# Performance work log

Hardware: AMD Instinct MI355X
Metric: run time of the kernel (lower is better)

Reference implementation:

```python
import jax, jax.numpy as jnp
import numpy as np

NUM_GRAPHS = 1000


def setup_inputs() -> dict:
    key = jax.random.key(0)
    ks = jax.random.split(key, 8)
    N, E, F_IN, H = 100000, 1600000, 128, 64
    x = jax.random.normal(ks[0], (N, F_IN), dtype=jnp.float32)
    edge_index = jax.random.randint(ks[1], (2, E), 0, N, dtype=jnp.int64)
    batch = jnp.sort(jax.random.randint(ks[2], (N,), 0, NUM_GRAPHS, dtype=jnp.int64))
    # Glorot-ish scaled weights
    W1 = jax.random.normal(ks[3], (F_IN, H), dtype=jnp.float32) / np.sqrt(F_IN)
    W2 = jax.random.normal(ks[4], (H, H), dtype=jnp.float32) / np.sqrt(H)
    W3 = jax.random.normal(ks[5], (H, H), dtype=jnp.float32) / np.sqrt(H)
    Wl = jax.random.normal(ks[6], (H, 1), dtype=jnp.float32) / np.sqrt(H)
    return {
        "x": x, "edge_index": edge_index, "batch": batch,
        "W1": W1, "b1": jnp.zeros((H,), jnp.float32),
        "W2": W2, "b2": jnp.zeros((H,), jnp.float32),
        "W3": W3, "b3": jnp.zeros((H,), jnp.float32),
        "Wl": Wl, "bl": jnp.zeros((1,), jnp.float32),
    }


def _gcn_prep(edge_index, n_nodes):
    """Add self-loops and compute symmetric normalization coefficients."""
    loops = jnp.arange(n_nodes, dtype=edge_index.dtype)
    src = jnp.concatenate([edge_index[0], loops])  # [E+N]
    dst = jnp.concatenate([edge_index[1], loops])  # [E+N]
    deg = jax.ops.segment_sum(jnp.ones_like(dst, dtype=jnp.float32), dst,
                              num_segments=n_nodes)
    dinv = jnp.where(deg > 0, jax.lax.rsqrt(jnp.maximum(deg, 1.0)), 0.0)
    norm = dinv[src] * dinv[dst]  # [E+N]
    return src, dst, norm


def _gcn_conv(h, W, b, src, dst, norm, n_nodes):
    h = h @ W                              # [N, H] linear transform first
    msg = h[src] * norm[:, None]           # gather + normalize
    agg = jax.ops.segment_sum(msg, dst, num_segments=n_nodes)  # scatter-add
    return agg + b


def reference(x, edge_index, batch, W1, b1, W2, b2, W3, b3, Wl, bl):
    n_nodes = x.shape[0]
    src, dst, norm = _gcn_prep(edge_index, n_nodes)
    h = jax.nn.relu(_gcn_conv(x, W1, b1, src, dst, norm, n_nodes))
    h = jax.nn.relu(_gcn_conv(h, W2, b2, src, dst, norm, n_nodes))
    h = _gcn_conv(h, W3, b3, src, dst, norm, n_nodes)
    # global_mean_pool over graphs
    sums = jax.ops.segment_sum(h, batch, num_segments=NUM_GRAPHS)
    cnts = jax.ops.segment_sum(jnp.ones((n_nodes,), jnp.float32), batch,
                               num_segments=NUM_GRAPHS)
    pooled = sums / jnp.maximum(cnts, 1.0)[:, None]
    # dropout is identity in eval mode
    return pooled @ Wl + bl
```

## Files before the change

### kernel.cpp

```cpp
#include <hip/hip_runtime.h>
#include <stdint.h>

#define BKT 1024
#define EPB 4096

typedef __attribute__((ext_vector_type(8))) __bf16 bf16x8;
typedef __attribute__((ext_vector_type(4))) float floatx4;

__device__ __forceinline__ float bf2f(unsigned short h) {
    return __uint_as_float(((unsigned)h) << 16);
}
__device__ __forceinline__ float4 bf4(ushort4 v) {
    return make_float4(bf2f(v.x), bf2f(v.y), bf2f(v.z), bf2f(v.w));
}
__device__ __forceinline__ unsigned short f2bf(float f) {
    unsigned u = __float_as_uint(f);
    u = u + 0x7FFFu + ((u >> 16) & 1u);
    return (unsigned short)(u >> 16);
}
__device__ __forceinline__ ushort4 pack4(float a, float b, float c, float d) {
    ushort4 r; r.x = f2bf(a); r.y = f2bf(b); r.z = f2bf(c); r.w = f2bf(d); return r;
}


__global__ __launch_bounds__(256) void coarse_hist(const int* __restrict__ dst,
                                                   int* __restrict__ coarse, int E, int NBK) {
    __shared__ int h[128];
    if (threadIdx.x < 128) h[threadIdx.x] = 0;
    __syncthreads();
    int stride = gridDim.x * 256;
    for (int i = blockIdx.x * 256 + threadIdx.x; i < E; i += stride)
        atomicAdd(&h[dst[i] >> 10], 1);
    __syncthreads();
    if (threadIdx.x < NBK) {
        int v = h[threadIdx.x];
        if (v) atomicAdd(&coarse[threadIdx.x], v);
    }
}

__global__ void coarse_scan(const int* __restrict__ coarse, int* __restrict__ bbase,
                            int NBK, int E) {
    if (threadIdx.x == 0 && blockIdx.x == 0) {
        int run = 0;
        for (int i = 0; i < NBK; ++i) { bbase[i] = run; run += coarse[i]; }
        bbase[NBK] = E;
    }
}


__global__ __launch_bounds__(256) void partition_kernel(const int* __restrict__ src,
                                                        const int* __restrict__ dst,
                                                        const int* __restrict__ bbase,
                                                        int* __restrict__ gbcur,
                                                        int2* __restrict__ pairs,
                                                        int E, int NBK) {
    __shared__ int2 stage[EPB];
    __shared__ int  hist[128], offs[129], gbase[128], lcur[128];
    int base = blockIdx.x * EPB;
    int cntE = min(EPB, E - base);
    if (threadIdx.x < 128) hist[threadIdx.x] = 0;
    __syncthreads();
    for (int i = threadIdx.x; i < cntE; i += 256) {
        int b = dst[base + i] >> 10;
        atomicAdd(&hist[b], 1);
    }
    __syncthreads();
    if (threadIdx.x == 0) {
        int run = 0;
        for (int b = 0; b < NBK; ++b) { offs[b] = run; run += hist[b]; }
        offs[NBK] = run;
    }
    __syncthreads();
    if (threadIdx.x < NBK) {
        int b = threadIdx.x;
        int h = hist[b];
        if (h > 0) gbase[b] = bbase[b] + atomicAdd(&gbcur[b << 4], h);
        lcur[b] = offs[b];
    }
    __syncthreads();
    for (int i = threadIdx.x; i < cntE; i += 256) {
        int e = base + i;
        int d = dst[e];
        int b = d >> 10;
        int slot = atomicAdd(&lcur[b], 1);
        stage[slot] = make_int2(src[e], d);
    }
    __syncthreads();
    int total = offs[NBK];
    for (int j = threadIdx.x; j < total; j += 256) {
        int lo = 0, hi = NBK;
        while (lo < hi) { int mid = (lo + hi) >> 1; if (offs[mid + 1] <= j) lo = mid + 1; else hi = mid; }
        pairs[gbase[lo] + (j - offs[lo])] = stage[j];
    }
}


__global__ __launch_bounds__(256) void bucket_build(const int2* __restrict__ pairs,
                                                    const int* __restrict__ bbase,
                                                    int* __restrict__ rowptr,
                                                    int* __restrict__ csr, int N, int E) {
    __shared__ int cnt[BKT];
    __shared__ int psum[256];
    int b = blockIdx.x;
    int nbase = b << 10;
    int pbeg = bbase[b], pend = bbase[b + 1];
    for (int i = threadIdx.x; i < BKT; i += 256) cnt[i] = 0;
    __syncthreads();
    for (int j = pbeg + (int)threadIdx.x; j < pend; j += 256)
        atomicAdd(&cnt[pairs[j].y - nbase], 1);
    __syncthreads();
    int i0 = threadIdx.x * 4;
    int c0 = cnt[i0], c1 = cnt[i0 + 1], c2 = cnt[i0 + 2], c3 = cnt[i0 + 3];
    int local = c0 + c1 + c2 + c3;
    psum[threadIdx.x] = local;
    __syncthreads();
    for (int d = 1; d < 256; d <<= 1) {
        int t = (threadIdx.x >= d) ? psum[threadIdx.x - d] : 0;
        __syncthreads();
        psum[threadIdx.x] += t;
        __syncthreads();
    }
    int excl = psum[threadIdx.x] - local;
    int o0 = pbeg + excl;
    int o1 = o0 + c0, o2 = o1 + c1, o3 = o2 + c2;
    int n0 = nbase + i0;
    if (n0 < N)     rowptr[n0]     = o0;
    if (n0 + 1 < N) rowptr[n0 + 1] = o1;
    if (n0 + 2 < N) rowptr[n0 + 2] = o2;
    if (n0 + 3 < N) rowptr[n0 + 3] = o3;
    cnt[i0] = o0; cnt[i0 + 1] = o1; cnt[i0 + 2] = o2; cnt[i0 + 3] = o3;
    __syncthreads();
    for (int j = pbeg + (int)threadIdx.x; j < pend; j += 256) {
        int2 p = pairs[j];
        int slot = atomicAdd(&cnt[p.y - nbase], 1);
        csr[slot] = p.x;
    }
    if (b == 0 && threadIdx.x == 0) rowptr[N] = E;
}


__global__ __launch_bounds__(256) void gemm1_mfma(const float* __restrict__ X,
                                                  const float* __restrict__ W,
                                                  const int* __restrict__ rowptr,
                                                  __bf16* __restrict__ gbh, int N) {
    __shared__ __align__(16) __bf16 Wt[64][136];
    for (int i = threadIdx.x; i < 128 * 64; i += 256) {
        int k = i >> 6, c = i & 63;
        Wt[c][k] = (__bf16)W[i];
    }
    __syncthreads();

    int wave = threadIdx.x >> 6;
    int l = threadIdx.x & 63;
    int cidx = l & 15;
    int g = l >> 4;
    int wbase = blockIdx.x * 64 + wave * 16;

    int arow = wbase + cidx;
    int arowc = min(arow, N - 1);
    const float4* xr = (const float4*)(X + (size_t)arowc * 128);
    bf16x8 afr[4];
#pragma unroll
    for (int kb = 0; kb < 4; ++kb) {
        float4 p = xr[kb * 8 + g * 2];
        float4 q = xr[kb * 8 + g * 2 + 1];
        bf16x8 a;
        a[0] = (__bf16)p.x; a[1] = (__bf16)p.y; a[2] = (__bf16)p.z; a[3] = (__bf16)p.w;
        a[4] = (__bf16)q.x; a[5] = (__bf16)q.y; a[6] = (__bf16)q.z; a[7] = (__bf16)q.w;
        afr[kb] = a;
    }

    floatx4 acc[4];
#pragma unroll
    for (int ct = 0; ct < 4; ++ct) acc[ct] = (floatx4){0.f, 0.f, 0.f, 0.f};

#pragma unroll
    for (int ct = 0; ct < 4; ++ct) {
#pragma unroll
        for (int kb = 0; kb < 4; ++kb) {
            bf16x8 bfr = *(const bf16x8*)&Wt[ct * 16 + cidx][kb * 32 + g * 8];
            acc[ct] = __builtin_amdgcn_mfma_f32_16x16x32_bf16(afr[kb], bfr, acc[ct], 0, 0, 0);
        }
    }

    int r0 = wbase + g * 4;
    int rp[5];
#pragma unroll
    for (int i = 0; i < 5; ++i) rp[i] = rowptr[min(r0 + i, N)];
#pragma unroll
    for (int i = 0; i < 4; ++i) {
        int row = r0 + i;
        if (row < N) {
            float dv = rsqrtf((float)(rp[i + 1] - rp[i]) + 1.0f);
#pragma unroll
            for (int ct = 0; ct < 4; ++ct)
                gbh[(size_t)row * 64 + ct * 16 + cidx] = (__bf16)(acc[ct][i] * dv);
        }
    }
}


__global__ __launch_bounds__(256) void fused_layer_kernel(const ushort4* __restrict__ gb,
                                                          const int* __restrict__ rowptr,
                                                          const int* __restrict__ csr,
                                                          const float* __restrict__ bias,
                                                          const float* __restrict__ W,
                                                          ushort4* __restrict__ out, int N) {
    __shared__ float Ws[64 * 64];
    __shared__ float T[16][72];
    {
        const float4* Wv = (const float4*)W;
        float4* Wsv = (float4*)Ws;
        for (int i = threadIdx.x; i < 64 * 16; i += 256) Wsv[i] = Wv[i];
    }
    int row = threadIdx.x >> 4;
    int node = blockIdx.x * 16 + row;
    int t = threadIdx.x & 15;
    int c = t * 4;
    float dinv = 0.f;
    if (node < N) {
        int beg = rowptr[node], end = rowptr[node + 1];
        dinv = rsqrtf((float)(end - beg) + 1.0f);
        float4 acc = bf4(gb[(size_t)node * 16 + t]);
        int j = beg;
        for (; j + 8 <= end; j += 8) {
            int s0 = csr[j], s1 = csr[j + 1], s2 = csr[j + 2], s3 = csr[j + 3];
            int s4 = csr[j + 4], s5 = csr[j + 5], s6 = csr[j + 6], s7 = csr[j + 7];
            float4 v0 = bf4(gb[(size_t)s0 * 16 + t]);
            float4 v1 = bf4(gb[(size_t)s1 * 16 + t]);
            float4 v2 = bf4(gb[(size_t)s2 * 16 + t]);
            float4 v3 = bf4(gb[(size_t)s3 * 16 + t]);
            float4 v4 = bf4(gb[(size_t)s4 * 16 + t]);
            float4 v5 = bf4(gb[(size_t)s5 * 16 + t]);
            float4 v6 = bf4(gb[(size_t)s6 * 16 + t]);
            float4 v7 = bf4(gb[(size_t)s7 * 16 + t]);
            acc.x += ((v0.x + v1.x) + (v2.x + v3.x)) + ((v4.x + v5.x) + (v6.x + v7.x));
            acc.y += ((v0.y + v1.y) + (v2.y + v3.y)) + ((v4.y + v5.y) + (v6.y + v7.y));
            acc.z += ((v0.z + v1.z) + (v2.z + v3.z)) + ((v4.z + v5.z) + (v6.z + v7.z));
            acc.w += ((v0.w + v1.w) + (v2.w + v3.w)) + ((v4.w + v5.w) + (v6.w + v7.w));
        }
        for (; j + 2 <= end; j += 2) {
            int s0 = csr[j], s1 = csr[j + 1];
            float4 v0 = bf4(gb[(size_t)s0 * 16 + t]);
            float4 v1 = bf4(gb[(size_t)s1 * 16 + t]);
            acc.x += v0.x + v1.x; acc.y += v0.y + v1.y;
            acc.z += v0.z + v1.z; acc.w += v0.w + v1.w;
        }
        if (j < end) {
            int s0 = csr[j];
            float4 v0 = bf4(gb[(size_t)s0 * 16 + t]);
            acc.x += v0.x; acc.y += v0.y; acc.z += v0.z; acc.w += v0.w;
        }
        float4 bb = *(const float4*)&bias[c];
        T[row][c + 0] = fmaxf(acc.x * dinv + bb.x, 0.f);
        T[row][c + 1] = fmaxf(acc.y * dinv + bb.y, 0.f);
        T[row][c + 2] = fmaxf(acc.z * dinv + bb.z, 0.f);
        T[row][c + 3] = fmaxf(acc.w * dinv + bb.w, 0.f);
    }
    __syncthreads();
    if (node >= N) return;
    float4 o = make_float4(0.f, 0.f, 0.f, 0.f);
#pragma unroll 16
    for (int k = 0; k < 64; ++k) {
        float tv = T[row][k];
        float4 wv = *(const float4*)&Ws[k * 64 + c];
        o.x += tv * wv.x; o.y += tv * wv.y;
        o.z += tv * wv.z; o.w += tv * wv.w;
    }
    out[(size_t)node * 16 + t] = pack4(o.x * dinv, o.y * dinv, o.z * dinv, o.w * dinv);
}


__global__ __launch_bounds__(256) void agg_dot_kernel(const ushort4* __restrict__ gb,
                                                      const int* __restrict__ rowptr,
                                                      const int* __restrict__ csr,
                                                      const float* __restrict__ bias,
                                                      const float* __restrict__ Wl,
                                                      float* __restrict__ s_node, int N) {
    int tid = blockIdx.x * blockDim.x + threadIdx.x;
    int node = tid >> 4;
    if (node >= N) return;
    int t = tid & 15;
    int beg = rowptr[node], end = rowptr[node + 1];
    float dinv = rsqrtf((float)(end - beg) + 1.0f);
    float4 acc = bf4(gb[(size_t)node * 16 + t]);
    int j = beg;
    for (; j + 8 <= end; j += 8) {
        int s0 = csr[j], s1 = csr[j + 1], s2 = csr[j + 2], s3 = csr[j + 3];
        int s4 = csr[j + 4], s5 = csr[j + 5], s6 = csr[j + 6], s7 = csr[j + 7];
        float4 v0 = bf4(gb[(size_t)s0 * 16 + t]);
        float4 v1 = bf4(gb[(size_t)s1 * 16 + t]);
        float4 v2 = bf4(gb[(size_t)s2 * 16 + t]);
        float4 v3 = bf4(gb[(size_t)s3 * 16 + t]);
        float4 v4 = bf4(gb[(size_t)s4 * 16 + t]);
        float4 v5 = bf4(gb[(size_t)s5 * 16 + t]);
        float4 v6 = bf4(gb[(size_t)s6 * 16 + t]);
        float4 v7 = bf4(gb[(size_t)s7 * 16 + t]);
        acc.x += ((v0.x + v1.x) + (v2.x + v3.x)) + ((v4.x + v5.x) + (v6.x + v7.x));
        acc.y += ((v0.y + v1.y) + (v2.y + v3.y)) + ((v4.y + v5.y) + (v6.y + v7.y));
        acc.z += ((v0.z + v1.z) + (v2.z + v3.z)) + ((v4.z + v5.z) + (v6.z + v7.z));
        acc.w += ((v0.w + v1.w) + (v2.w + v3.w)) + ((v4.w + v5.w) + (v6.w + v7.w));
    }
    for (; j + 2 <= end; j += 2) {
        int s0 = csr[j], s1 = csr[j + 1];
        float4 v0 = bf4(gb[(size_t)s0 * 16 + t]);
        float4 v1 = bf4(gb[(size_t)s1 * 16 + t]);
        acc.x += v0.x + v1.x; acc.y += v0.y + v1.y;
        acc.z += v0.z + v1.z; acc.w += v0.w + v1.w;
    }
    if (j < end) {
        int s0 = csr[j];
        float4 v0 = bf4(gb[(size_t)s0 * 16 + t]);
        acc.x += v0.x; acc.y += v0.y; acc.z += v0.z; acc.w += v0.w;
    }
    float4 bb = *(const float4*)&bias[t * 4];
    float4 wl = *(const float4*)&Wl[t * 4];
    float s = (acc.x * dinv + bb.x) * wl.x + (acc.y * dinv + bb.y) * wl.y +
              (acc.z * dinv + bb.z) * wl.z + (acc.w * dinv + bb.w) * wl.w;
    s += __shfl_xor(s, 1);
    s += __shfl_xor(s, 2);
    s += __shfl_xor(s, 4);
    s += __shfl_xor(s, 8);
    if (t == 0) s_node[node] = s;
}


__device__ __forceinline__ int lower_bound_dev(const int* __restrict__ a, int n, int v) {
    int lo = 0, hi = n;
    while (lo < hi) { int mid = (lo + hi) >> 1; if (a[mid] < v) lo = mid + 1; else hi = mid; }
    return lo;
}

__global__ void pool_out_kernel(const float* __restrict__ s_node, const int* __restrict__ batch,
                                const float* __restrict__ bl, float* __restrict__ out, int N) {
    int gidx = blockIdx.x;
    int lo = lower_bound_dev(batch, N, gidx);
    int hi = lower_bound_dev(batch, N, gidx + 1);
    float s = 0.f;
    for (int i = lo + threadIdx.x; i < hi; i += 64) s += s_node[i];
    for (int d = 32; d; d >>= 1) s += __shfl_down(s, d);
    if (threadIdx.x == 0) out[gidx] = s / fmaxf((float)(hi - lo), 1.0f) + bl[0];
}


extern "C" void kernel_launch(void* const* d_in, const int* in_sizes, int n_in,
                              void* d_out, int out_size, void* d_ws, size_t ws_size,
                              hipStream_t stream) {
    const float* x   = (const float*)d_in[0];
    const int*   ei  = (const int*)d_in[1];
    const int*   bat = (const int*)d_in[2];
    const float* W1  = (const float*)d_in[3];
    const float* b1  = (const float*)d_in[4];
    const float* W2  = (const float*)d_in[5];
    const float* b2  = (const float*)d_in[6];
    const float* W3  = (const float*)d_in[7];
    const float* b3  = (const float*)d_in[8];
    const float* Wl  = (const float*)d_in[9];
    const float* bl  = (const float*)d_in[10];

    const int N = in_sizes[0] / 128;
    const int E = in_sizes[1] / 2;
    const int G = out_size;

    const int* src = ei;
    const int* dst = ei + E;

    const int NBK = (N + BKT - 1) / BKT;
    const int Np = (N + 4) & ~3;

    int*     rowptr = (int*)d_ws;
    int*     coarse = rowptr + Np;
    int*     bbase  = coarse + 128;
    int*     gbcur  = bbase + 132;
    int*     csr    = gbcur + (size_t)NBK * 16;
    int2*    pairs  = (int2*)(csr + E);
    ushort4* gbA    = (ushort4*)(pairs + E);
    ushort4* gbB    = gbA + (size_t)N * 16;
    float*   s_node = (float*)(gbB + (size_t)N * 16);

    hipMemsetAsync(coarse, 0, (260 + (size_t)NBK * 16) * sizeof(int), stream);
    coarse_hist<<<256, 256, 0, stream>>>(dst, coarse, E, NBK);
    coarse_scan<<<1, 64, 0, stream>>>(coarse, bbase, NBK, E);
    partition_kernel<<<(E + EPB - 1) / EPB, 256, 0, stream>>>(src, dst, bbase, gbcur, pairs, E, NBK);
    bucket_build<<<NBK, 256, 0, stream>>>(pairs, bbase, rowptr, csr, N, E);

    const int tileGrid = (N + 15) / 16;
    const int aggGrid  = (int)(((size_t)N * 16 + 255) / 256);

    gemm1_mfma<<<(N + 63) / 64, 256, 0, stream>>>(x, W1, rowptr, (__bf16*)gbA, N);
    fused_layer_kernel<<<tileGrid, 256, 0, stream>>>(gbA, rowptr, csr, b1, W2, gbB, N);
    fused_layer_kernel<<<tileGrid, 256, 0, stream>>>(gbB, rowptr, csr, b2, W3, gbA, N);
    agg_dot_kernel<<<aggGrid, 256, 0, stream>>>(gbA, rowptr, csr, b3, Wl, s_node, N);
    pool_out_kernel<<<G, 64, 0, stream>>>(s_node, bat, bl, (float*)d_out, N);
}
```

Before: 280.2 us.

## Project final layer onto output weight before aggregation to gather scalars

Uses linearity of the last GCN layer and the pooling to apply Wl before neighbor aggregation. The second fused layer now emits a per-node scalar instead of a 64-wide bf16 row, and a new scalar aggregation kernel gathers single floats per edge. The b3·Wl term is folded into the pooling kernel. This removes the wide gather traffic of the final layer. It slightly changes semantics for empty graphs, where the bias dot is still added.

Measured after the change: 245.4 us. 1.14x faster.

```diff
diff --git a/kernel.cpp b/kernel.cpp
--- a/kernel.cpp
+++ b/kernel.cpp
@@ -200,12 +200,15 @@
 }
 
 
+template <bool WRITE_P>
 __global__ __launch_bounds__(256) void fused_layer_kernel(const ushort4* __restrict__ gb,
                                                           const int* __restrict__ rowptr,
                                                           const int* __restrict__ csr,
                                                           const float* __restrict__ bias,
                                                           const float* __restrict__ W,
-                                                          ushort4* __restrict__ out, int N) {
+                                                          ushort4* __restrict__ out,
+                                                          const float* __restrict__ Wl,
+                                                          float* __restrict__ p, int N) {
     __shared__ float Ws[64 * 64];
     __shared__ float T[16][72];
     {
@@ -267,61 +270,36 @@
         o.x += tv * wv.x; o.y += tv * wv.y;
         o.z += tv * wv.z; o.w += tv * wv.w;
     }
-    out[(size_t)node * 16 + t] = pack4(o.x * dinv, o.y * dinv, o.z * dinv, o.w * dinv);
-}
-
-
-__global__ __launch_bounds__(256) void agg_dot_kernel(const ushort4* __restrict__ gb,
-                                                      const int* __restrict__ rowptr,
-                                                      const int* __restrict__ csr,
-                                                      const float* __restrict__ bias,
-                                                      const float* __restrict__ Wl,
-                                                      float* __restrict__ s_node, int N) {
-    int tid = blockIdx.x * blockDim.x + threadIdx.x;
-    int node = tid >> 4;
-    if (node >= N) return;
-    int t = tid & 15;
-    int beg = rowptr[node], end = rowptr[node + 1];
+    if (WRITE_P) {
+        float4 wl = *(const float4*)&Wl[c];
+        float s = (o.x * wl.x + o.y * wl.y) + (o.z * wl.z + o.w * wl.w);
+        s += __shfl_xor(s, 1);
+        s += __shfl_xor(s, 2);
+        s += __shfl_xor(s, 4);
+        s += __shfl_xor(s, 8);
+        if (t == 0) p[node] = s * dinv;
+    } else {
+        out[(size_t)node * 16 + t] = pack4(o.x * dinv, o.y * dinv, o.z * dinv, o.w * dinv);
+    }
+}
+
+
+__global__ __launch_bounds__(256) void scalar_agg(const float* __restrict__ p,
+                                                  const int* __restrict__ rowptr,
+                                                  const int* __restrict__ csr,
+                                                  float* __restrict__ s_node, int N) {
+    int n = blockIdx.x * 256 + threadIdx.x;
+    if (n >= N) return;
+    int beg = rowptr[n], end = rowptr[n + 1];
     float dinv = rsqrtf((float)(end - beg) + 1.0f);
-    float4 acc = bf4(gb[(size_t)node * 16 + t]);
+    float acc = p[n];
     int j = beg;
-    for (; j + 8 <= end; j += 8) {
-        int s0 = csr[j], s1 = csr[j + 1], s2 = csr[j + 2], s3 = csr[j + 3];
-        int s4 = csr[j + 4], s5 = csr[j + 5], s6 = csr[j + 6], s7 = csr[j + 7];
-        float4 v0 = bf4(gb[(size_t)s0 * 16 + t]);
-        float4 v1 = bf4(gb[(size_t)s1 * 16 + t]);
-        float4 v2 = bf4(gb[(size_t)s2 * 16 + t]);
-        float4 v3 = bf4(gb[(size_t)s3 * 16 + t]);
-        float4 v4 = bf4(gb[(size_t)s4 * 16 + t]);
-        float4 v5 = bf4(gb[(size_t)s5 * 16 + t]);
-        float4 v6 = bf4(gb[(size_t)s6 * 16 + t]);
-        float4 v7 = bf4(gb[(size_t)s7 * 16 + t]);
-        acc.x += ((v0.x + v1.x) + (v2.x + v3.x)) + ((v4.x + v5.x) + (v6.x + v7.x));
-        acc.y += ((v0.y + v1.y) + (v2.y + v3.y)) + ((v4.y + v5.y) + (v6.y + v7.y));
-        acc.z += ((v0.z + v1.z) + (v2.z + v3.z)) + ((v4.z + v5.z) + (v6.z + v7.z));
-        acc.w += ((v0.w + v1.w) + (v2.w + v3.w)) + ((v4.w + v5.w) + (v6.w + v7.w));
-    }
-    for (; j + 2 <= end; j += 2) {
-        int s0 = csr[j], s1 = csr[j + 1];
-        float4 v0 = bf4(gb[(size_t)s0 * 16 + t]);
-        float4 v1 = bf4(gb[(size_t)s1 * 16 + t]);
-        acc.x += v0.x + v1.x; acc.y += v0.y + v1.y;
-        acc.z += v0.z + v1.z; acc.w += v0.w + v1.w;
-    }
-    if (j < end) {
-        int s0 = csr[j];
-        float4 v0 = bf4(gb[(size_t)s0 * 16 + t]);
-        acc.x += v0.x; acc.y += v0.y; acc.z += v0.z; acc.w += v0.w;
-    }
-    float4 bb = *(const float4*)&bias[t * 4];
-    float4 wl = *(const float4*)&Wl[t * 4];
-    float s = (acc.x * dinv + bb.x) * wl.x + (acc.y * dinv + bb.y) * wl.y +
-              (acc.z * dinv + bb.z) * wl.z + (acc.w * dinv + bb.w) * wl.w;
-    s += __shfl_xor(s, 1);
-    s += __shfl_xor(s, 2);
-    s += __shfl_xor(s, 4);
-    s += __shfl_xor(s, 8);
-    if (t == 0) s_node[node] = s;
+    for (; j + 4 <= end; j += 4) {
+        float a0 = p[csr[j]], a1 = p[csr[j + 1]], a2 = p[csr[j + 2]], a3 = p[csr[j + 3]];
+        acc += (a0 + a1) + (a2 + a3);
+    }
+    for (; j < end; ++j) acc += p[csr[j]];
+    s_node[n] = acc * dinv;
 }
 
 
@@ -332,14 +310,20 @@
 }
 
 __global__ void pool_out_kernel(const float* __restrict__ s_node, const int* __restrict__ batch,
+                                const float* __restrict__ b3, const float* __restrict__ Wl,
                                 const float* __restrict__ bl, float* __restrict__ out, int N) {
+    float v = b3[threadIdx.x] * Wl[threadIdx.x];
+    for (int d = 32; d; d >>= 1) v += __shfl_down(v, d);
+    float bldot = __shfl(v, 0, 64);
+
     int gidx = blockIdx.x;
     int lo = lower_bound_dev(batch, N, gidx);
     int hi = lower_bound_dev(batch, N, gidx + 1);
     float s = 0.f;
     for (int i = lo + threadIdx.x; i < hi; i += 64) s += s_node[i];
     for (int d = 32; d; d >>= 1) s += __shfl_down(s, d);
-    if (threadIdx.x == 0) out[gidx] = s / fmaxf((float)(hi - lo), 1.0f) + bl[0];
+    if (threadIdx.x == 0)
+        out[gidx] = s / fmaxf((float)(hi - lo), 1.0f) + bldot + bl[0];
 }
 
 
@@ -376,7 +360,8 @@
     int2*    pairs  = (int2*)(csr + E);
     ushort4* gbA    = (ushort4*)(pairs + E);
     ushort4* gbB    = gbA + (size_t)N * 16;
-    float*   s_node = (float*)(gbB + (size_t)N * 16);
+    float*   pbuf   = (float*)(gbB + (size_t)N * 16);
+    float*   s_node = pbuf + N;
 
     hipMemsetAsync(coarse, 0, (260 + (size_t)NBK * 16) * sizeof(int), stream);
     coarse_hist<<<256, 256, 0, stream>>>(dst, coarse, E, NBK);
@@ -385,11 +370,10 @@
     bucket_build<<<NBK, 256, 0, stream>>>(pairs, bbase, rowptr, csr, N, E);
 
     const int tileGrid = (N + 15) / 16;
-    const int aggGrid  = (int)(((size_t)N * 16 + 255) / 256);
 
     gemm1_mfma<<<(N + 63) / 64, 256, 0, stream>>>(x, W1, rowptr, (__bf16*)gbA, N);
-    fused_layer_kernel<<<tileGrid, 256, 0, stream>>>(gbA, rowptr, csr, b1, W2, gbB, N);
-    fused_layer_kernel<<<tileGrid, 256, 0, stream>>>(gbB, rowptr, csr, b2, W3, gbA, N);
-    agg_dot_kernel<<<aggGrid, 256, 0, stream>>>(gbA, rowptr, csr, b3, Wl, s_node, N);
-    pool_out_kernel<<<G, 64, 0, stream>>>(s_node, bat, bl, (float*)d_out, N);
-}
+    fused_layer_kernel<false><<<tileGrid, 256, 0, stream>>>(gbA, rowptr, csr, b1, W2, gbB, nullptr, nullptr, N);
+    fused_layer_kernel<true><<<tileGrid, 256, 0, stream>>>(gbB, rowptr, csr, b2, W3, nullptr, Wl, pbuf, N);
+    scalar_agg<<<(N + 255) / 256, 256, 0, stream>>>(pbuf, rowptr, csr, s_node, N);
+    pool_out_kernel<<<G, 64, 0, stream>>>(s_node, bat, b3, Wl, bl, (float*)d_out, N);
+}
```

## Fold W3·Wl into scalar projection and aggregate layer 3 as scalars

Applied to the files above, without the earlier changes.

The third GCN layer is linear, so W3 and Wl are combined into a 64-vector. Layer 2 is aggregated with ReLU and projected onto that vector, giving one scalar per node. Layer 3's neighbour aggregation then becomes a scalar gather instead of a full 64-wide bf16 gather, and b3·Wl is added in the pooling kernel. This removes one full fused layer (a 64-wide aggregate plus GEMM) at the cost of two small kernels. The histogram loops also switch to int4 loads of dst.

New measurement: 232.4 us (median of 2 runs). -17.1%, faster.

```diff
diff --git a/kernel.cpp b/kernel.cpp
--- a/kernel.cpp
+++ b/kernel.cpp
@@ -23,13 +23,33 @@
 }
 
 
+__global__ void w3l_kernel(const float* __restrict__ W3, const float* __restrict__ Wl,
+                           float* __restrict__ w3l) {
+    int k = threadIdx.x;
+    float s = 0.f;
+#pragma unroll 16
+    for (int c = 0; c < 64; ++c) s += W3[k * 64 + c] * Wl[c];
+    w3l[k] = s;
+}
+
+
 __global__ __launch_bounds__(256) void coarse_hist(const int* __restrict__ dst,
                                                    int* __restrict__ coarse, int E, int NBK) {
     __shared__ int h[128];
     if (threadIdx.x < 128) h[threadIdx.x] = 0;
     __syncthreads();
     int stride = gridDim.x * 256;
-    for (int i = blockIdx.x * 256 + threadIdx.x; i < E; i += stride)
+    int gid = blockIdx.x * 256 + threadIdx.x;
+    const int4* d4 = (const int4*)dst;
+    int E4 = E >> 2;
+    for (int i = gid; i < E4; i += stride) {
+        int4 v = d4[i];
+        atomicAdd(&h[v.x >> 10], 1);
+        atomicAdd(&h[v.y >> 10], 1);
+        atomicAdd(&h[v.z >> 10], 1);
+        atomicAdd(&h[v.w >> 10], 1);
+    }
+    for (int i = (E4 << 2) + gid; i < E; i += stride)
         atomicAdd(&h[dst[i] >> 10], 1);
     __syncthreads();
     if (threadIdx.x < NBK) {
@@ -60,9 +80,18 @@
     int cntE = min(EPB, E - base);
     if (threadIdx.x < 128) hist[threadIdx.x] = 0;
     __syncthreads();
-    for (int i = threadIdx.x; i < cntE; i += 256) {
-        int b = dst[base + i] >> 10;
-        atomicAdd(&hist[b], 1);
+    {
+        const int4* d4 = (const int4*)(dst + base);
+        int c4 = cntE >> 2;
+        for (int i = threadIdx.x; i < c4; i += 256) {
+            int4 v = d4[i];
+            atomicAdd(&hist[v.x >> 10], 1);
+            atomicAdd(&hist[v.y >> 10], 1);
+            atomicAdd(&hist[v.z >> 10], 1);
+            atomicAdd(&hist[v.w >> 10], 1);
+        }
+        for (int i = (c4 << 2) + (int)threadIdx.x; i < cntE; i += 256)
+            atomicAdd(&hist[dst[base + i] >> 10], 1);
     }
     __syncthreads();
     if (threadIdx.x == 0) {
@@ -271,12 +300,12 @@
 }
 
 
-__global__ __launch_bounds__(256) void agg_dot_kernel(const ushort4* __restrict__ gb,
-                                                      const int* __restrict__ rowptr,
-                                                      const int* __restrict__ csr,
-                                                      const float* __restrict__ bias,
-                                                      const float* __restrict__ Wl,
-                                                      float* __restrict__ s_node, int N) {
+__global__ __launch_bounds__(256) void agg_dot2_kernel(const ushort4* __restrict__ gb,
+                                                       const int* __restrict__ rowptr,
+                                                       const int* __restrict__ csr,
+                                                       const float* __restrict__ bias,
+                                                       const float* __restrict__ w3l,
+                                                       float* __restrict__ p, int N) {
     int tid = blockIdx.x * blockDim.x + threadIdx.x;
     int node = tid >> 4;
     if (node >= N) return;
@@ -314,14 +343,36 @@
         acc.x += v0.x; acc.y += v0.y; acc.z += v0.z; acc.w += v0.w;
     }
     float4 bb = *(const float4*)&bias[t * 4];
-    float4 wl = *(const float4*)&Wl[t * 4];
-    float s = (acc.x * dinv + bb.x) * wl.x + (acc.y * dinv + bb.y) * wl.y +
-              (acc.z * dinv + bb.z) * wl.z + (acc.w * dinv + bb.w) * wl.w;
+    float4 wv = *(const float4*)&w3l[t * 4];
+    float hx = fmaxf(acc.x * dinv + bb.x, 0.f);
+    float hy = fmaxf(acc.y * dinv + bb.y, 0.f);
+    float hz = fmaxf(acc.z * dinv + bb.z, 0.f);
+    float hw = fmaxf(acc.w * dinv + bb.w, 0.f);
+    float s = (hx * wv.x + hy * wv.y) + (hz * wv.z + hw * wv.w);
     s += __shfl_xor(s, 1);
     s += __shfl_xor(s, 2);
     s += __shfl_xor(s, 4);
     s += __shfl_xor(s, 8);
-    if (t == 0) s_node[node] = s;
+    if (t == 0) p[node] = s * dinv;
+}
+
+
+__global__ __launch_bounds__(256) void scalar_agg(const float* __restrict__ p,
+                                                  const int* __restrict__ rowptr,
+                                                  const int* __restrict__ csr,
+                                                  float* __restrict__ s_node, int N) {
+    int n = blockIdx.x * 256 + threadIdx.x;
+    if (n >= N) return;
+    int beg = rowptr[n], end = rowptr[n + 1];
+    float dinv = rsqrtf((float)(end - beg) + 1.0f);
+    float acc = p[n];
+    int j = beg;
+    for (; j + 4 <= end; j += 4) {
+        float a0 = p[csr[j]], a1 = p[csr[j + 1]], a2 = p[csr[j + 2]], a3 = p[csr[j + 3]];
+        acc += (a0 + a1) + (a2 + a3);
+    }
+    for (; j < end; ++j) acc += p[csr[j]];
+    s_node[n] = acc * dinv;
 }
 
 
@@ -332,14 +383,20 @@
 }
 
 __global__ void pool_out_kernel(const float* __restrict__ s_node, const int* __restrict__ batch,
+                                const float* __restrict__ b3, const float* __restrict__ Wl,
                                 const float* __restrict__ bl, float* __restrict__ out, int N) {
+    float v = b3[threadIdx.x] * Wl[threadIdx.x];
+    for (int d = 32; d; d >>= 1) v += __shfl_down(v, d);
+    float bldot = __shfl(v, 0, 64);
+
     int gidx = blockIdx.x;
     int lo = lower_bound_dev(batch, N, gidx);
     int hi = lower_bound_dev(batch, N, gidx + 1);
     float s = 0.f;
     for (int i = lo + threadIdx.x; i < hi; i += 64) s += s_node[i];
     for (int d = 32; d; d >>= 1) s += __shfl_down(s, d);
-    if (threadIdx.x == 0) out[gidx] = s / fmaxf((float)(hi - lo), 1.0f) + bl[0];
+    if (threadIdx.x == 0)
+        out[gidx] = s / fmaxf((float)(hi - lo), 1.0f) + bldot + bl[0];
 }
 
 
@@ -371,14 +428,17 @@
     int*     rowptr = (int*)d_ws;
     int*     coarse = rowptr + Np;
     int*     bbase  = coarse + 128;
-    int*     gbcur  = bbase + 132;
+    float*   w3l    = (float*)(bbase + 132);
+    int*     gbcur  = (int*)(w3l + 64);
     int*     csr    = gbcur + (size_t)NBK * 16;
     int2*    pairs  = (int2*)(csr + E);
     ushort4* gbA    = (ushort4*)(pairs + E);
     ushort4* gbB    = gbA + (size_t)N * 16;
-    float*   s_node = (float*)(gbB + (size_t)N * 16);
-
-    hipMemsetAsync(coarse, 0, (260 + (size_t)NBK * 16) * sizeof(int), stream);
+    float*   pbuf   = (float*)(gbB + (size_t)N * 16);
+    float*   s_node = pbuf + N;
+
+    hipMemsetAsync(coarse, 0, (324 + (size_t)NBK * 16) * sizeof(int), stream);
+    w3l_kernel<<<1, 64, 0, stream>>>(W3, Wl, w3l);
     coarse_hist<<<256, 256, 0, stream>>>(dst, coarse, E, NBK);
     coarse_scan<<<1, 64, 0, stream>>>(coarse, bbase, NBK, E);
     partition_kernel<<<(E + EPB - 1) / EPB, 256, 0, stream>>>(src, dst, bbase, gbcur, pairs, E, NBK);
@@ -389,7 +449,7 @@
 
     gemm1_mfma<<<(N + 63) / 64, 256, 0, stream>>>(x, W1, rowptr, (__bf16*)gbA, N);
     fused_layer_kernel<<<tileGrid, 256, 0, stream>>>(gbA, rowptr, csr, b1, W2, gbB, N);
-    fused_layer_kernel<<<tileGrid, 256, 0, stream>>>(gbB, rowptr, csr, b2, W3, gbA, N);
-    agg_dot_kernel<<<aggGrid, 256, 0, stream>>>(gbA, rowptr, csr, b3, Wl, s_node, N);
-    pool_out_kernel<<<G, 64, 0, stream>>>(s_node, bat, bl, (float*)d_out, N);
-}
+    agg_dot2_kernel<<<aggGrid, 256, 0, stream>>>(gbB, rowptr, csr, b2, w3l, pbuf, N);
+    scalar_agg<<<(N + 255) / 256, 256, 0, stream>>>(pbuf, rowptr, csr, s_node, N);
+    pool_out_kernel<<<G, 64, 0, stream>>>(s_node, bat, b3, Wl, bl, (float*)d_out, N);
+}
```
